# Optimization experiments

Measured on AMD Instinct MI355X. Metric: run time of the kernel, lower is better.

## Reference

```python
import jax, jax.numpy as jnp
import numpy as np

D_REDUCE = 32
# combination indices (i<j), lexicographic, matching torch.combinations
_IDX_I, _IDX_J = np.triu_indices(D_REDUCE, k=1)


def setup_inputs() -> dict:
    key = jax.random.key(0)
    ks = jax.random.split(key, 5)
    B, L, d_model, d_red = 8, 4096, 1024, D_REDUCE
    plucker_dim = d_red * (d_red - 1) // 2  # 496
    return {
        "h": jax.random.normal(ks[0], (B, L, d_model), dtype=jnp.float32),
        "window_offset": 1,
        "W_red_w": jax.random.normal(ks[1], (d_model, d_red), dtype=jnp.float32) * (1.0 / np.sqrt(d_model)),
        "W_red_b": jax.random.normal(ks[2], (d_red,), dtype=jnp.float32) * 0.01,
        "W_plu_w": jax.random.normal(ks[3], (plucker_dim, d_model), dtype=jnp.float32) * (1.0 / np.sqrt(plucker_dim)),
        "W_plu_b": jax.random.normal(ks[4], (d_model,), dtype=jnp.float32) * 0.01,
    }


def reference(h, window_offset, W_red_w, W_red_b, W_plu_w, W_plu_b):
    B, L, d_model = h.shape
    delta = int(window_offset)
    if delta >= L:
        return jnp.zeros_like(h)
    idx_i = jnp.asarray(_IDX_I)
    idx_j = jnp.asarray(_IDX_J)
    # reduce: (B, L, d_red)
    z = jnp.einsum("bld,dr->blr", h, W_red_w) + W_red_b
    z_t = z[:, delta:, :]        # (B, L-delta, d_red)
    z_td = z[:, : L - delta, :]  # (B, L-delta, d_red)
    # Plucker coordinates: p_ij = z_t[i]*z_td[j] - z_t[j]*z_td[i]  -> (B, L-delta, 496)
    p = z_t[..., idx_i] * z_td[..., idx_j] - z_t[..., idx_j] * z_td[..., idx_i]
    norm = jnp.sqrt(jnp.sum(p * p, axis=-1, keepdims=True))
    p_hat = p / jnp.maximum(norm, 1e-8)
    g_valid = jnp.einsum("blp,pd->bld", p_hat, W_plu_w) + W_plu_b
    g = jnp.zeros((B, L, d_model), dtype=h.dtype)
    g = g.at[:, delta:, :].set(g_valid)
    return g
```

## Files before the change

### kernel.cpp

```cpp
#include <hip/hip_runtime.h>
#include <hip/hip_bf16.h>

#define L_SEQ  4096
#define NBATCH 8
#define DMODEL 1024
#define DRED   32
#define NPAIR  496
#define PK     512
#define MROWS  (NBATCH * L_SEQ)

typedef __bf16 bf16x8 __attribute__((ext_vector_type(8)));
typedef float  f32x4  __attribute__((ext_vector_type(4)));
typedef unsigned short u16x8 __attribute__((ext_vector_type(8)));

typedef const __attribute__((address_space(1))) void g_void;
typedef __attribute__((address_space(3))) void lds_void;

struct PairTab { unsigned short v[512]; };
static constexpr PairTab make_tab() {
  PairTab t{};
  int p = 0;
  for (int i = 0; i < DRED; ++i)
    for (int j = i + 1; j < DRED; ++j) { t.v[p] = (unsigned short)(i | (j << 8)); ++p; }
  for (; p < 512; ++p) t.v[p] = 0;
  return t;
}
__constant__ PairTab PTAB = make_tab();

__global__ __launch_bounds__(256) void ktransW(const float* __restrict__ Wplu,
                                               __bf16* __restrict__ Wt) {
  __shared__ float tile[64][65];
  const int k0 = (blockIdx.x & 7) << 6;
  const int n0 = (blockIdx.x >> 3) << 6;
  const int tid = threadIdx.x;
#pragma unroll
  for (int it = 0; it < 16; ++it) {
    int e = it * 256 + tid;
    int i = e >> 6, j = e & 63;
    float v = 0.f;
    if (k0 + i < NPAIR) v = Wplu[(size_t)(k0 + i) * DMODEL + n0 + j];
    tile[i][j] = v;
  }
  __syncthreads();
#pragma unroll
  for (int it = 0; it < 16; ++it) {
    int e = it * 256 + tid;
    int rn = e >> 6, ck = e & 63;
    Wt[(size_t)(n0 + rn) * PK + k0 + ck] = (__bf16)tile[ck][rn];
  }
}

__global__ __launch_bounds__(256) void kprepWz(const float* __restrict__ Wred,
                                               __bf16* __restrict__ Bh,
                                               __bf16* __restrict__ Bl) {
  int idx = blockIdx.x * 256 + threadIdx.x;
  int n = idx >> 10, k = idx & 1023;
  float v = Wred[k * DRED + n];
  __bf16 hh = (__bf16)v;
  Bh[idx] = hh;
  Bl[idx] = (__bf16)(v - (float)hh);
}

__global__ __launch_bounds__(256) void kz(const float* __restrict__ h,
                                          const __bf16* __restrict__ Bh,
                                          const __bf16* __restrict__ Bl,
                                          const float* __restrict__ Wrb,
                                          float* __restrict__ z) {
  const int w = threadIdx.x >> 6;
  const int lane = threadIdx.x & 63;
  const int l15 = lane & 15, hi = lane >> 4;
  const int m0 = blockIdx.x * 64 + w * 16;
  f32x4 acc[2] = {};
  const float* hp = h + (size_t)(m0 + l15) * DMODEL + hi * 8;
  const __bf16* bh0 = Bh + (size_t)l15 * DMODEL + hi * 8;
  const __bf16* bh1 = bh0 + 16 * DMODEL;
  const __bf16* bl0 = Bl + (size_t)l15 * DMODEL + hi * 8;
  const __bf16* bl1 = bl0 + 16 * DMODEL;
#pragma unroll 8
  for (int kt = 0; kt < 32; ++kt) {
    const int ko = kt * 32;
    f32x4 v0 = *(const f32x4*)(hp + ko);
    f32x4 v1 = *(const f32x4*)(hp + ko + 4);
    bf16x8 ah, al;
#pragma unroll
    for (int q = 0; q < 4; ++q) {
      float f0 = v0[q], f1 = v1[q];
      __bf16 h0 = (__bf16)f0, h1 = (__bf16)f1;
      ah[q] = h0;     ah[q + 4] = h1;
      al[q] = (__bf16)(f0 - (float)h0);
      al[q + 4] = (__bf16)(f1 - (float)h1);
    }
    bf16x8 b0h = *(const bf16x8*)(bh0 + ko);
    bf16x8 b1h = *(const bf16x8*)(bh1 + ko);
    bf16x8 b0l = *(const bf16x8*)(bl0 + ko);
    bf16x8 b1l = *(const bf16x8*)(bl1 + ko);
    acc[0] = __builtin_amdgcn_mfma_f32_16x16x32_bf16(ah, b0h, acc[0], 0, 0, 0);
    acc[1] = __builtin_amdgcn_mfma_f32_16x16x32_bf16(ah, b1h, acc[1], 0, 0, 0);
    acc[0] = __builtin_amdgcn_mfma_f32_16x16x32_bf16(al, b0h, acc[0], 0, 0, 0);
    acc[1] = __builtin_amdgcn_mfma_f32_16x16x32_bf16(al, b1h, acc[1], 0, 0, 0);
    acc[0] = __builtin_amdgcn_mfma_f32_16x16x32_bf16(ah, b0l, acc[0], 0, 0, 0);
    acc[1] = __builtin_amdgcn_mfma_f32_16x16x32_bf16(ah, b1l, acc[1], 0, 0, 0);
  }
#pragma unroll
  for (int nt = 0; nt < 2; ++nt) {
    const float bias = Wrb[nt * 16 + l15];
#pragma unroll
    for (int q = 0; q < 4; ++q) {
      z[(size_t)(m0 + hi * 4 + q) * DRED + nt * 16 + l15] = acc[nt][q] + bias;
    }
  }
}

__global__ __launch_bounds__(256) void kpairs(const float* __restrict__ z,
                                              const int* __restrict__ dOff,
                                              __bf16* __restrict__ A) {
  const int delta = *dOff;
  const int lane = threadIdx.x & 63;
  const int m = blockIdx.x * 4 + (threadIdx.x >> 6);
  const int t = m & (L_SEQ - 1);
  __bf16* arow = A + (size_t)m * PK;
  if (t < delta) {
    u16x8 zz = {0, 0, 0, 0, 0, 0, 0, 0};
    *(u16x8*)(arow + lane * 8) = zz;
    return;
  }
  const float zt  = z[(size_t)m * DRED + (lane & 31)];
  const float ztd = z[(size_t)(m - delta) * DRED + (lane & 31)];
  const u16x8 tab = *(const u16x8*)(PTAB.v + lane * 8);
  float p[8];
  float s = 0.f;
#pragma unroll
  for (int q = 0; q < 8; ++q) {
    const int i = tab[q] & 255;
    const int j = tab[q] >> 8;
    float zti  = __shfl(zt,  i, 64);
    float ztdj = __shfl(ztd, j, 64);
    float ztj  = __shfl(zt,  j, 64);
    float ztdi = __shfl(ztd, i, 64);
    p[q] = fmaf(zti, ztdj, -(ztj * ztdi));
    s = fmaf(p[q], p[q], s);
  }
#pragma unroll
  for (int off = 1; off < 64; off <<= 1) s += __shfl_xor(s, off, 64);
  const float rcp = 1.f / fmaxf(sqrtf(s), 1e-8f);
  bf16x8 o;
#pragma unroll
  for (int q = 0; q < 8; ++q) o[q] = (__bf16)(p[q] * rcp);
  *(bf16x8*)(arow + lane * 8) = o;
}

__global__ __launch_bounds__(256) void kgemm(const __bf16* __restrict__ A,
                                             const __bf16* __restrict__ Bt,
                                             const float* __restrict__ bias,
                                             const int* __restrict__ dOff,
                                             float* __restrict__ out) {
  __shared__ __bf16 Asm[2][128 * 32];
  __shared__ __bf16 Bsm[2][128 * 32];
  const int delta = *dOff;
  const int d = blockIdx.x;
  const int lb = ((d & 7) << 8) + (d >> 3);
  const int bm = lb >> 3, bn = lb & 7;
  const int m0 = bm << 7, n0 = bn << 7;
  const int t = threadIdx.x;
  const int wv = t >> 6, lane = t & 63;
  const int l15 = lane & 15, hi = lane >> 4;
  const int wm = (wv >> 1) << 6, wn = (wv & 1) << 6;

  f32x4 acc[4][4] = {};

  const int r0 = t >> 2,         jsw0 = (t & 3) ^ (r0 & 3);
  const int r1 = (t + 256) >> 2, jsw1 = (t & 3) ^ (r1 & 3);
  const __bf16* gA0 = A  + (size_t)(m0 + r0) * PK + jsw0 * 8;
  const __bf16* gA1 = A  + (size_t)(m0 + r1) * PK + jsw1 * 8;
  const __bf16* gB0 = Bt + (size_t)(n0 + r0) * PK + jsw0 * 8;
  const __bf16* gB1 = Bt + (size_t)(n0 + r1) * PK + jsw1 * 8;
  const int cb0 = (wv << 6) * 16;
  const int cb1 = (256 + (wv << 6)) * 16;

#define STAGE(buf, kt) do {                                                          \
    const int _ko = (kt) * 32;                                                       \
    __builtin_amdgcn_global_load_lds((g_void*)(gA0 + _ko),                           \
        (lds_void*)((char*)Asm[buf] + cb0), 16, 0, 0);                               \
    __builtin_amdgcn_global_load_lds((g_void*)(gA1 + _ko),                           \
        (lds_void*)((char*)Asm[buf] + cb1), 16, 0, 0);                               \
    __builtin_amdgcn_global_load_lds((g_void*)(gB0 + _ko),                           \
        (lds_void*)((char*)Bsm[buf] + cb0), 16, 0, 0);                               \
    __builtin_amdgcn_global_load_lds((g_void*)(gB1 + _ko),                           \
        (lds_void*)((char*)Bsm[buf] + cb1), 16, 0, 0);                               \
  } while (0)

  STAGE(0, 0);
  __syncthreads();
  int buf = 0;
  for (int kt = 0; kt < 16; ++kt) {
    if (kt < 15) STAGE(buf ^ 1, kt + 1);
    bf16x8 afr[4], bfr[4];
#pragma unroll
    for (int mi = 0; mi < 4; ++mi) {
      const int row = wm + mi * 16 + l15;
      const int jj = hi ^ (row & 3);
      afr[mi] = *(const bf16x8*)((const char*)Asm[buf] + row * 64 + jj * 16);
    }
#pragma unroll
    for (int ni = 0; ni < 4; ++ni) {
      const int row = wn + ni * 16 + l15;
      const int jj = hi ^ (row & 3);
      bfr[ni] = *(const bf16x8*)((const char*)Bsm[buf] + row * 64 + jj * 16);
    }
#pragma unroll
    for (int mi = 0; mi < 4; ++mi)
#pragma unroll
      for (int ni = 0; ni < 4; ++ni)
        acc[mi][ni] = __builtin_amdgcn_mfma_f32_16x16x32_bf16(afr[mi], bfr[ni],
                                                              acc[mi][ni], 0, 0, 0);
    __syncthreads();
    buf ^= 1;
  }
#undef STAGE

  float bv[4];
#pragma unroll
  for (int ni = 0; ni < 4; ++ni) bv[ni] = bias[n0 + wn + ni * 16 + l15];
#pragma unroll
  for (int mi = 0; mi < 4; ++mi)
#pragma unroll
    for (int ni = 0; ni < 4; ++ni)
#pragma unroll
      for (int q = 0; q < 4; ++q) {
        const int row = m0 + wm + mi * 16 + hi * 4 + q;
        const int col = n0 + wn + ni * 16 + l15;
        float v = acc[mi][ni][q] + bv[ni];
        if ((row & (L_SEQ - 1)) < delta) v = 0.f;
        out[(size_t)row * DMODEL + col] = v;
      }
}

extern "C" void kernel_launch(void* const* d_in, const int* in_sizes, int n_in,
                              void* d_out, int out_size, void* d_ws, size_t ws_size,
                              hipStream_t stream) {
  const float* h    = (const float*)d_in[0];
  const int*   woff = (const int*)d_in[1];
  const float* Wred = (const float*)d_in[2];
  const float* Wrb  = (const float*)d_in[3];
  const float* Wplu = (const float*)d_in[4];
  const float* Wpb  = (const float*)d_in[5];
  float* out = (float*)d_out;

  char* ws = (char*)d_ws;
  float*  z   = (float*)ws;
  __bf16* Aph = (__bf16*)(ws + (4u << 20));
  __bf16* Wt  = (__bf16*)(ws + (36u << 20));
  __bf16* Bh  = (__bf16*)(ws + (37u << 20));
  __bf16* Bl  = (__bf16*)(ws + (37u << 20) + (64u << 10));

  hipLaunchKernelGGL(ktransW,  dim3(128),        dim3(256), 0, stream, Wplu, Wt);
  hipLaunchKernelGGL(kprepWz,  dim3(128),        dim3(256), 0, stream, Wred, Bh, Bl);
  hipLaunchKernelGGL(kz,       dim3(MROWS / 64), dim3(256), 0, stream, h, Bh, Bl, Wrb, z);
  hipLaunchKernelGGL(kpairs,   dim3(MROWS / 4),  dim3(256), 0, stream, z, woff, Aph);
  hipLaunchKernelGGL(kgemm,    dim3(2048),       dim3(256), 0, stream, Aph, Wt, Wpb, woff, out);
}
```

Before: 132.9 us.

## Merge prep kernels, double rows per wave in kz, stage GEMM epilogue through LDS

Folds the two weight-prep kernels into one launch to save a kernel launch. kz now has each wave compute 32 rows, halving the grid and reusing the W_red fragment loads across two row groups. The GEMM epilogue writes each 16x64 tile into a per-wave LDS scratch buffer and reads it back so the output goes out as 16-byte vector stores instead of scalar strided stores. The trade-off is 16KB of extra LDS per block, which may lower GEMM occupancy, plus more registers in kz.

Result: faster. 126.4 us (-4.9%).

```diff
diff --git a/kernel.cpp b/kernel.cpp
--- a/kernel.cpp
+++ b/kernel.cpp
@@ -27,38 +27,42 @@
 }
 __constant__ PairTab PTAB = make_tab();
 
-__global__ __launch_bounds__(256) void ktransW(const float* __restrict__ Wplu,
-                                               __bf16* __restrict__ Wt) {
-  __shared__ float tile[64][65];
-  const int k0 = (blockIdx.x & 7) << 6;
-  const int n0 = (blockIdx.x >> 3) << 6;
+__global__ __launch_bounds__(256) void kprep(const float* __restrict__ Wplu,
+                                             __bf16* __restrict__ Wt,
+                                             const float* __restrict__ Wred,
+                                             __bf16* __restrict__ Bh,
+                                             __bf16* __restrict__ Bl) {
   const int tid = threadIdx.x;
-#pragma unroll
-  for (int it = 0; it < 16; ++it) {
-    int e = it * 256 + tid;
-    int i = e >> 6, j = e & 63;
-    float v = 0.f;
-    if (k0 + i < NPAIR) v = Wplu[(size_t)(k0 + i) * DMODEL + n0 + j];
-    tile[i][j] = v;
-  }
-  __syncthreads();
-#pragma unroll
-  for (int it = 0; it < 16; ++it) {
-    int e = it * 256 + tid;
-    int rn = e >> 6, ck = e & 63;
-    Wt[(size_t)(n0 + rn) * PK + k0 + ck] = (__bf16)tile[ck][rn];
-  }
-}
-
-__global__ __launch_bounds__(256) void kprepWz(const float* __restrict__ Wred,
-                                               __bf16* __restrict__ Bh,
-                                               __bf16* __restrict__ Bl) {
-  int idx = blockIdx.x * 256 + threadIdx.x;
-  int n = idx >> 10, k = idx & 1023;
-  float v = Wred[k * DRED + n];
-  __bf16 hh = (__bf16)v;
-  Bh[idx] = hh;
-  Bl[idx] = (__bf16)(v - (float)hh);
+  if (blockIdx.x < 128) {
+    __shared__ float tile[64][65];
+    const int k0 = (blockIdx.x & 7) << 6;
+    const int n0 = (blockIdx.x >> 3) << 6;
+#pragma unroll
+    for (int it = 0; it < 16; ++it) {
+      int e = it * 256 + tid;
+      int i = e >> 6, j = e & 63;
+      float v = 0.f;
+      if (k0 + i < NPAIR) v = Wplu[(size_t)(k0 + i) * DMODEL + n0 + j];
+      tile[i][j] = v;
+    }
+    __syncthreads();
+#pragma unroll
+    for (int it = 0; it < 16; ++it) {
+      int e = it * 256 + tid;
+      int rn = e >> 6, ck = e & 63;
+      Wt[(size_t)(n0 + rn) * PK + k0 + ck] = (__bf16)tile[ck][rn];
+    }
+  } else {
+#pragma unroll
+    for (int e = 0; e < 2; ++e) {
+      int idx = (blockIdx.x - 128) * 512 + e * 256 + tid;
+      int n = idx >> 10, k = idx & 1023;
+      float v = Wred[k * DRED + n];
+      __bf16 hh = (__bf16)v;
+      Bh[idx] = hh;
+      Bl[idx] = (__bf16)(v - (float)hh);
+    }
+  }
 }
 
 __global__ __launch_bounds__(256) void kz(const float* __restrict__ h,
@@ -69,46 +73,57 @@
   const int w = threadIdx.x >> 6;
   const int lane = threadIdx.x & 63;
   const int l15 = lane & 15, hi = lane >> 4;
-  const int m0 = blockIdx.x * 64 + w * 16;
-  f32x4 acc[2] = {};
-  const float* hp = h + (size_t)(m0 + l15) * DMODEL + hi * 8;
+  const int m0 = blockIdx.x * 128 + w * 32;
+  f32x4 acc[2][2] = {};
+  const float* hp0 = h + (size_t)(m0 + l15) * DMODEL + hi * 8;
+  const float* hp1 = hp0 + (size_t)16 * DMODEL;
   const __bf16* bh0 = Bh + (size_t)l15 * DMODEL + hi * 8;
   const __bf16* bh1 = bh0 + 16 * DMODEL;
   const __bf16* bl0 = Bl + (size_t)l15 * DMODEL + hi * 8;
   const __bf16* bl1 = bl0 + 16 * DMODEL;
-#pragma unroll 8
+#pragma unroll 4
   for (int kt = 0; kt < 32; ++kt) {
     const int ko = kt * 32;
-    f32x4 v0 = *(const f32x4*)(hp + ko);
-    f32x4 v1 = *(const f32x4*)(hp + ko + 4);
-    bf16x8 ah, al;
-#pragma unroll
-    for (int q = 0; q < 4; ++q) {
-      float f0 = v0[q], f1 = v1[q];
-      __bf16 h0 = (__bf16)f0, h1 = (__bf16)f1;
-      ah[q] = h0;     ah[q + 4] = h1;
-      al[q] = (__bf16)(f0 - (float)h0);
-      al[q + 4] = (__bf16)(f1 - (float)h1);
+    bf16x8 ah[2], al[2];
+#pragma unroll
+    for (int rg = 0; rg < 2; ++rg) {
+      const float* hp = rg ? hp1 : hp0;
+      f32x4 v0 = *(const f32x4*)(hp + ko);
+      f32x4 v1 = *(const f32x4*)(hp + ko + 4);
+#pragma unroll
+      for (int q = 0; q < 4; ++q) {
+        float f0 = v0[q], f1 = v1[q];
+        __bf16 h0 = (__bf16)f0, h1 = (__bf16)f1;
+        ah[rg][q] = h0;     ah[rg][q + 4] = h1;
+        al[rg][q] = (__bf16)(f0 - (float)h0);
+        al[rg][q + 4] = (__bf16)(f1 - (float)h1);
+      }
     }
     bf16x8 b0h = *(const bf16x8*)(bh0 + ko);
     bf16x8 b1h = *(const bf16x8*)(bh1 + ko);
     bf16x8 b0l = *(const bf16x8*)(bl0 + ko);
     bf16x8 b1l = *(const bf16x8*)(bl1 + ko);
-    acc[0] = __builtin_amdgcn_mfma_f32_16x16x32_bf16(ah, b0h, acc[0], 0, 0, 0);
-    acc[1] = __builtin_amdgcn_mfma_f32_16x16x32_bf16(ah, b1h, acc[1], 0, 0, 0);
-    acc[0] = __builtin_amdgcn_mfma_f32_16x16x32_bf16(al, b0h, acc[0], 0, 0, 0);
-    acc[1] = __builtin_amdgcn_mfma_f32_16x16x32_bf16(al, b1h, acc[1], 0, 0, 0);
-    acc[0] = __builtin_amdgcn_mfma_f32_16x16x32_bf16(ah, b0l, acc[0], 0, 0, 0);
-    acc[1] = __builtin_amdgcn_mfma_f32_16x16x32_bf16(ah, b1l, acc[1], 0, 0, 0);
-  }
-#pragma unroll
-  for (int nt = 0; nt < 2; ++nt) {
-    const float bias = Wrb[nt * 16 + l15];
-#pragma unroll
-    for (int q = 0; q < 4; ++q) {
-      z[(size_t)(m0 + hi * 4 + q) * DRED + nt * 16 + l15] = acc[nt][q] + bias;
-    }
-  }
+#pragma unroll
+    for (int rg = 0; rg < 2; ++rg) {
+      acc[rg][0] = __builtin_amdgcn_mfma_f32_16x16x32_bf16(ah[rg], b0h, acc[rg][0], 0, 0, 0);
+      acc[rg][1] = __builtin_amdgcn_mfma_f32_16x16x32_bf16(ah[rg], b1h, acc[rg][1], 0, 0, 0);
+      acc[rg][0] = __builtin_amdgcn_mfma_f32_16x16x32_bf16(al[rg], b0h, acc[rg][0], 0, 0, 0);
+      acc[rg][1] = __builtin_amdgcn_mfma_f32_16x16x32_bf16(al[rg], b1h, acc[rg][1], 0, 0, 0);
+      acc[rg][0] = __builtin_amdgcn_mfma_f32_16x16x32_bf16(ah[rg], b0l, acc[rg][0], 0, 0, 0);
+      acc[rg][1] = __builtin_amdgcn_mfma_f32_16x16x32_bf16(ah[rg], b1l, acc[rg][1], 0, 0, 0);
+    }
+  }
+#pragma unroll
+  for (int rg = 0; rg < 2; ++rg)
+#pragma unroll
+    for (int nt = 0; nt < 2; ++nt) {
+      const float bias = Wrb[nt * 16 + l15];
+#pragma unroll
+      for (int q = 0; q < 4; ++q) {
+        z[(size_t)(m0 + rg * 16 + hi * 4 + q) * DRED + nt * 16 + l15]
+            = acc[rg][nt][q] + bias;
+      }
+    }
 }
 
 __global__ __launch_bounds__(256) void kpairs(const float* __restrict__ z,
@@ -156,6 +171,7 @@
                                              float* __restrict__ out) {
   __shared__ __bf16 Asm[2][128 * 32];
   __shared__ __bf16 Bsm[2][128 * 32];
+  __shared__ __align__(16) float scr_all[4][1024];
   const int delta = *dOff;
   const int d = blockIdx.x;
   const int lb = ((d & 7) << 8) + (d >> 3);
@@ -165,6 +181,7 @@
   const int wv = t >> 6, lane = t & 63;
   const int l15 = lane & 15, hi = lane >> 4;
   const int wm = (wv >> 1) << 6, wn = (wv & 1) << 6;
+  float* scr = scr_all[wv];
 
   f32x4 acc[4][4] = {};
 
@@ -222,17 +239,24 @@
 #pragma unroll
   for (int ni = 0; ni < 4; ++ni) bv[ni] = bias[n0 + wn + ni * 16 + l15];
 #pragma unroll
-  for (int mi = 0; mi < 4; ++mi)
+  for (int mi = 0; mi < 4; ++mi) {
 #pragma unroll
     for (int ni = 0; ni < 4; ++ni)
 #pragma unroll
       for (int q = 0; q < 4; ++q) {
-        const int row = m0 + wm + mi * 16 + hi * 4 + q;
-        const int col = n0 + wn + ni * 16 + l15;
+        const int r16 = hi * 4 + q;
         float v = acc[mi][ni][q] + bv[ni];
-        if ((row & (L_SEQ - 1)) < delta) v = 0.f;
-        out[(size_t)row * DMODEL + col] = v;
+        if (((m0 + wm + mi * 16 + r16) & (L_SEQ - 1)) < delta) v = 0.f;
+        scr[r16 * 64 + ni * 16 + l15] = v;
       }
+#pragma unroll
+    for (int e = 0; e < 4; ++e) {
+      const int r16 = e * 4 + hi;
+      f32x4 vv = *(const f32x4*)(scr + r16 * 64 + l15 * 4);
+      *(f32x4*)(out + (size_t)(m0 + wm + mi * 16 + r16) * DMODEL
+                    + n0 + wn + l15 * 4) = vv;
+    }
+  }
 }
 
 extern "C" void kernel_launch(void* const* d_in, const int* in_sizes, int n_in,
@@ -253,9 +277,8 @@
   __bf16* Bh  = (__bf16*)(ws + (37u << 20));
   __bf16* Bl  = (__bf16*)(ws + (37u << 20) + (64u << 10));
 
-  hipLaunchKernelGGL(ktransW,  dim3(128),        dim3(256), 0, stream, Wplu, Wt);
-  hipLaunchKernelGGL(kprepWz,  dim3(128),        dim3(256), 0, stream, Wred, Bh, Bl);
-  hipLaunchKernelGGL(kz,       dim3(MROWS / 64), dim3(256), 0, stream, h, Bh, Bl, Wrb, z);
-  hipLaunchKernelGGL(kpairs,   dim3(MROWS / 4),  dim3(256), 0, stream, z, woff, Aph);
-  hipLaunchKernelGGL(kgemm,    dim3(2048),       dim3(256), 0, stream, Aph, Wt, Wpb, woff, out);
-}
+  hipLaunchKernelGGL(kprep,  dim3(192),         dim3(256), 0, stream, Wplu, Wt, Wred, Bh, Bl);
+  hipLaunchKernelGGL(kz,     dim3(MROWS / 128), dim3(256), 0, stream, h, Bh, Bl, Wrb, z);
+  hipLaunchKernelGGL(kpairs, dim3(MROWS / 4),   dim3(256), 0, stream, z, woff, Aph);
+  hipLaunchKernelGGL(kgemm,  dim3(2048),        dim3(256), 0, stream, Aph, Wt, Wpb, woff, out);
+}
```
